# Performance work log

Measured on AMD Instinct MI355X. Metric: run time of the kernel, lower is better.

Reference implementation:

```python
import jax, jax.numpy as jnp
import numpy as np

N_SLOTS, WORD, R_HEADS = 256, 64, 4
EPS = 1e-6
IFACE = R_HEADS * WORD + 3 * WORD + 5 * R_HEADS + 3  # 471


def _oneplus(x):
    return 1.0 + jax.nn.softplus(x)


def _content_weights(M, k, beta):
    # M: (B,N,W), k: (B,H,W), beta: (B,H) -> (B,H,N) softmax over slots
    Mn = M / (jnp.linalg.norm(M, axis=-1, keepdims=True) + EPS)
    kn = k / (jnp.linalg.norm(k, axis=-1, keepdims=True) + EPS)
    sim = jnp.einsum('bnw,bhw->bhn', Mn, kn)
    return jax.nn.softmax(beta[..., None] * sim, axis=-1)


def setup_inputs() -> dict:
    key = jax.random.key(0)
    ks = jax.random.split(key, 6)
    T, B, I, H, O = 64, 16, 512, 512, 512
    nn_in = I + R_HEADS * WORD  # 768
    return {
        'x': jax.random.normal(ks[0], (T, B, I), jnp.float32),
        'W_hid': jax.random.normal(ks[1], (nn_in, H), jnp.float32) / np.sqrt(nn_in),
        'b_hid': jnp.zeros((H,), jnp.float32),
        'W_iface': jax.random.normal(ks[2], (H, IFACE), jnp.float32) / np.sqrt(H),
        'W_out': jax.random.normal(ks[3], (H, O), jnp.float32) / np.sqrt(H),
        'W_memout': jax.random.normal(ks[4], (R_HEADS * WORD, O), jnp.float32) / np.sqrt(R_HEADS * WORD),
    }


def reference(x, W_hid, b_hid, W_iface, W_out, W_memout):
    T, B, _ = x.shape
    N, Wd, R = N_SLOTS, WORD, R_HEADS
    sizes = [R * Wd, R, Wd, 1, Wd, Wd, R, 1, 1, 3 * R]
    splits = np.cumsum(sizes)[:-1]
    eye = jnp.eye(N, dtype=x.dtype)

    def step(carry, x_t):
        M, u, p, L, ww, rw, rv = carry
        nn_in = jnp.concatenate([x_t, rv.reshape(B, R * Wd)], axis=-1)
        h = jax.nn.relu(nn_in @ W_hid + b_hid)
        pre_out = h @ W_out
        iface = h @ W_iface
        rk, rb, wk, wb, ev, wv, fg, ag, wg, rm = jnp.split(iface, splits, axis=-1)
        rk = rk.reshape(B, R, Wd)
        rb = _oneplus(rb)                       # (B,R)
        wk = wk.reshape(B, 1, Wd)
        wb = _oneplus(wb)                       # (B,1)
        ev = jax.nn.sigmoid(ev)                 # (B,Wd)
        fg = jax.nn.sigmoid(fg)                 # (B,R)
        ag = jax.nn.sigmoid(ag)                 # (B,1)
        wg = jax.nn.sigmoid(wg)                 # (B,1)
        rm = jax.nn.softmax(rm.reshape(B, R, 3), axis=-1)
        # --- usage / retention ---
        ret = jnp.prod(1.0 - fg[:, :, None] * rw, axis=1)          # (B,N)
        u_new = (u + ww - u * ww) * ret
        # --- allocation via usage sort ---
        free = jnp.argsort(u_new, axis=1)                           # ascending usage
        su = jnp.take_along_axis(u_new, free, axis=1)
        cp = jnp.cumprod(jnp.concatenate([jnp.ones((B, 1), su.dtype), su[:, :-1]], axis=1), axis=1)
        a_sorted = (1.0 - su) * cp
        inv = jnp.argsort(free, axis=1)
        a = jnp.take_along_axis(a_sorted, inv, axis=1)              # (B,N)
        # --- write weighting + memory update ---
        cw = _content_weights(M, wk, wb)[:, 0]                      # (B,N)
        ww_new = wg * (ag * a + (1.0 - ag) * cw)                    # (B,N)
        M_new = M * (1.0 - ww_new[:, :, None] * ev[:, None, :]) + ww_new[:, :, None] * wv[:, None, :]
        # --- temporal link matrix ---
        L_new = (1.0 - ww_new[:, :, None] - ww_new[:, None, :]) * L + ww_new[:, :, None] * p[:, None, :]
        L_new = L_new * (1.0 - eye)
        p_new = (1.0 - jnp.sum(ww_new, axis=1, keepdims=True)) * p + ww_new
        # --- read ---
        rc = _content_weights(M_new, rk, rb)                        # (B,R,N)
        fwd = jnp.einsum('bnm,brm->brn', L_new, rw)
        bwd = jnp.einsum('bmn,brm->brn', L_new, rw)
        rw_new = rm[:, :, 0:1] * bwd + rm[:, :, 1:2] * rc + rm[:, :, 2:3] * fwd
        rv_new = jnp.einsum('bnw,brn->brw', M_new, rw_new)          # (B,R,Wd)
        out = pre_out + rv_new.reshape(B, R * Wd) @ W_memout
        return (M_new, u_new, p_new, L_new, ww_new, rw_new, rv_new), out

    init = (jnp.full((B, N, Wd), 1e-6, x.dtype),
            jnp.zeros((B, N), x.dtype),
            jnp.zeros((B, N), x.dtype),
            jnp.zeros((B, N, N), x.dtype),
            jnp.zeros((B, N), x.dtype),
            jnp.zeros((B, R, N), x.dtype),
            jnp.zeros((B, R, Wd), x.dtype))
    _, outputs = jax.lax.scan(step, init, x)
    return outputs  # (T, B, output_size)
```

## Files before the change

### kernel.cpp

```cpp
#include <hip/hip_runtime.h>
#include <math.h>

#define TS 64
#define IFACE_N 471
#define EPS_ 1e-6f

#define OFF_RK 0
#define OFF_RB 256
#define OFF_WK 260
#define OFF_WB 324
#define OFF_EV 325
#define OFF_WV 389
#define OFF_FG 453
#define OFF_AG 457
#define OFF_WG 458
#define OFF_RM 459

#define O_HX   0
#define O_RS   524288
#define O_L    1048576
#define WIPS 260
#define WHPS 132
#define O_WIP  2097152
#define O_WHP  2219612

__device__ __forceinline__ float sigmoidf_(float x){ return 1.f/(1.f+expf(-x)); }
__device__ __forceinline__ float oneplusf_(float x){ return 1.f+fmaxf(x,0.f)+log1pf(expf(-fabsf(x))); }
__device__ __forceinline__ float wsum_(float v){
#pragma unroll
  for(int off=32; off>0; off>>=1) v += __shfl_xor(v,off,64);
  return v;
}
__device__ __forceinline__ float wmax_(float v){
#pragma unroll
  for(int off=32; off>0; off>>=1) v = fmaxf(v,__shfl_xor(v,off,64));
  return v;
}
__device__ __forceinline__ unsigned bf16rne_(float f){
  unsigned u = __float_as_uint(f);
  return (u + 0x7FFFu + ((u >> 16) & 1u)) >> 16;
}
__device__ __forceinline__ unsigned bf16pack_(float lo, float hi){
  return bf16rne_(lo) | (bf16rne_(hi) << 16);
}
__device__ __forceinline__ float bflo_(unsigned p){ return __uint_as_float(p << 16); }
__device__ __forceinline__ float bfhi_(unsigned p){ return __uint_as_float(p & 0xFFFF0000u); }

__device__ __forceinline__ float dot8_(uint4 p, const float* a, float acc){
  acc = fmaf(a[0], bflo_(p.x), acc); acc = fmaf(a[1], bfhi_(p.x), acc);
  acc = fmaf(a[2], bflo_(p.y), acc); acc = fmaf(a[3], bfhi_(p.y), acc);
  acc = fmaf(a[4], bflo_(p.z), acc); acc = fmaf(a[5], bfhi_(p.z), acc);
  acc = fmaf(a[6], bflo_(p.w), acc); acc = fmaf(a[7], bfhi_(p.w), acc);
  return acc;
}

__global__ void __launch_bounds__(256) kInit(float* ws){
  int g = blockIdx.x*256 + threadIdx.x;
  for (int i=g;i<1048576;i+=65536) ws[O_L+i]=0.f;
}

__global__ void __launch_bounds__(256)
kConv(const float* __restrict__ W_hid, const float* __restrict__ W_iface,
      float* __restrict__ ws)
{
  unsigned* Wip = (unsigned*)(ws + O_WIP);
  unsigned* Whp = (unsigned*)(ws + O_WHP);
  int g = blockIdx.x*256 + threadIdx.x;
  for (int i = g; i < 471*256; i += 65536) {
    int c = i >> 8, kp = i & 255;
    Wip[c*WIPS + kp] = bf16pack_(W_iface[(size_t)(2*kp)*IFACE_N + c],
                                 W_iface[(size_t)(2*kp+1)*IFACE_N + c]);
  }
  {
    int c = g >> 7, kp = g & 127;
    Whp[c*WHPS + kp] = bf16pack_(W_hid[(size_t)(512 + 2*kp)*512 + c],
                                 W_hid[(size_t)(513 + 2*kp)*512 + c]);
  }
}

__global__ void __launch_bounds__(256)
kPre(const float* __restrict__ x, const float* __restrict__ W_hid,
     const float* __restrict__ b_hid, float* __restrict__ ws)
{
  const int tid = threadIdx.x, blk = blockIdx.x;
  const int r0 = (blk >> 1) * 8, col = (blk & 1) * 256 + tid;
  __shared__ float xs[8][512];
  for (int i = tid; i < 8*512; i += 256) {
    int rr = i >> 9, k = i & 511;
    xs[rr][k] = x[(size_t)(r0+rr)*512 + k];
  }
  __syncthreads();
  float a0=0,a1=0,a2=0,a3=0,a4=0,a5=0,a6=0,a7=0;
  const float* Wp = W_hid + col;
#pragma unroll 4
  for (int k = 0; k < 512; k++) {
    float w = Wp[(size_t)k*512];
    a0 = fmaf(xs[0][k], w, a0); a1 = fmaf(xs[1][k], w, a1);
    a2 = fmaf(xs[2][k], w, a2); a3 = fmaf(xs[3][k], w, a3);
    a4 = fmaf(xs[4][k], w, a4); a5 = fmaf(xs[5][k], w, a5);
    a6 = fmaf(xs[6][k], w, a6); a7 = fmaf(xs[7][k], w, a7);
  }
  float bh = b_hid[col];
  float av[8] = {a0,a1,a2,a3,a4,a5,a6,a7};
#pragma unroll
  for (int i = 0; i < 8; i++)
    ws[O_HX + (size_t)(r0+i)*512 + col] = av[i] + bh;
}

__global__ void __launch_bounds__(1024, 4)
kLoop(const unsigned* __restrict__ WipT, const unsigned* __restrict__ WhpT,
      float* __restrict__ hx, float* __restrict__ rvs, float* __restrict__ Lall)
{
  const int tid = threadIdx.x, b = blockIdx.x;
  const int wv = tid >> 6, lane = tid & 63;

  __shared__ float hl[512];
  __shared__ float ifcl[480];
  __shared__ float psum[1024];
  __shared__ alignas(16) float ul[256];
  __shared__ alignas(16) float pOl[256];
  __shared__ float pNl[256];
  __shared__ alignas(16) float wwl[256];
  __shared__ alignas(16) float rwl[1024];
  __shared__ float wkn[64], rknl[256];
  __shared__ alignas(16) float evl[64], wvl[64];
  __shared__ float ssorted[256];
  __shared__ int   sidx[256];
  __shared__ float sal[256], siml[256], cwl[256];
  __shared__ float fwdl[1024], bwdl[1024], rcs[1024];
  __shared__ alignas(16) float bb[16][2][260];
  __shared__ float rvl[256];
  __shared__ float sSa;
  __shared__ alignas(16) float Ml[16384];

  float* Lg = Lall + (size_t)b*65536;

  if (tid < 512) hl[tid] = fmaxf(hx[(size_t)b*512 + tid], 0.f);
  rwl[tid] = 0.f;
  if (tid < 256){ ul[tid]=0.f; pOl[tid]=0.f; wwl[tid]=0.f; }
  for (int i = tid; i < 16384; i += 1024) Ml[i] = 1e-6f;
  __syncthreads();

  for (int t = 0; t < TS; t++) {
    if (tid < 512) hx[(size_t)(t*16 + b)*512 + tid] = hl[tid];

    {
      int col = tid & 511, kseg = tid >> 9;
      float acc = 0.f;
      if (col < IFACE_N) {
        const uint4* Wp = (const uint4*)(WipT + col*WIPS + kseg*128);
        const float* hp = hl + kseg*256;
#pragma unroll 8
        for (int q4 = 0; q4 < 32; q4++) acc = dot8_(Wp[q4], hp + q4*8, acc);
      }
      psum[tid] = acc;
    }
    __syncthreads();
    if (tid < IFACE_N) ifcl[tid] = psum[tid] + psum[512+tid];
    __syncthreads();

    if (tid < 256) {
      float ret = 1.f;
#pragma unroll
      for (int r = 0; r < 4; r++) {
        float fg = sigmoidf_(ifcl[OFF_FG + r]);
        ret *= (1.f - fg * rwl[r*256 + tid]);
      }
      float uo = ul[tid], wo = wwl[tid];
      ul[tid] = (uo + wo - uo*wo) * ret;
    } else if (tid >= 448 && tid < 512) {
      float kv = ifcl[OFF_WK + lane];
      float ss = wsum_(kv*kv);
      wkn[lane] = kv / (sqrtf(ss) + EPS_);
    } else if (tid >= 512 && tid < 768) {
      int r = wv - 8;
      float kv = ifcl[OFF_RK + r*64 + lane];
      float ss = wsum_(kv*kv);
      rknl[r*64 + lane] = kv / (sqrtf(ss) + EPS_);
    } else if (tid >= 768 && tid < 832) {
      evl[lane] = sigmoidf_(ifcl[OFF_EV + lane]);
    } else if (tid >= 832 && tid < 896) {
      wvl[lane] = ifcl[OFF_WV + lane];
    }
    __syncthreads();

    {
      int n = tid >> 2, q = tid & 3;
      const float4* Mp = (const float4*)(Ml + n*64 + q*16);
      float4 m0 = Mp[0], m1 = Mp[1], m2 = Mp[2], m3 = Mp[3];
      float un = ul[n];
      const float4* sp4 = (const float4*)(ul + q*64);
      int cnt = 0;
#pragma unroll 4
      for (int m4 = 0; m4 < 16; m4++) {
        float4 um = sp4[m4];
        int gm = q*64 + m4*4;
        cnt += (um.x < un || (um.x == un && gm   < n)) ? 1 : 0;
        cnt += (um.y < un || (um.y == un && gm+1 < n)) ? 1 : 0;
        cnt += (um.z < un || (um.z == un && gm+2 < n)) ? 1 : 0;
        cnt += (um.w < un || (um.w == un && gm+3 < n)) ? 1 : 0;
      }
      cnt += __shfl_xor(cnt, 1, 64);
      cnt += __shfl_xor(cnt, 2, 64);
      const float* kp = wkn + q*16;
      float ss = m0.x*m0.x + m0.y*m0.y + m0.z*m0.z + m0.w*m0.w
               + m1.x*m1.x + m1.y*m1.y + m1.z*m1.z + m1.w*m1.w
               + m2.x*m2.x + m2.y*m2.y + m2.z*m2.z + m2.w*m2.w
               + m3.x*m3.x + m3.y*m3.y + m3.z*m3.z + m3.w*m3.w;
      float dt = m0.x*kp[0] + m0.y*kp[1] + m0.z*kp[2] + m0.w*kp[3]
               + m1.x*kp[4] + m1.y*kp[5] + m1.z*kp[6] + m1.w*kp[7]
               + m2.x*kp[8] + m2.y*kp[9] + m2.z*kp[10] + m2.w*kp[11]
               + m3.x*kp[12] + m3.y*kp[13] + m3.z*kp[14] + m3.w*kp[15];
      ss += __shfl_xor(ss,1,64); ss += __shfl_xor(ss,2,64);
      dt += __shfl_xor(dt,1,64); dt += __shfl_xor(dt,2,64);
      if (q == 0) {
        ssorted[cnt] = un; sidx[cnt] = n;
        float wb = oneplusf_(ifcl[OFF_WB]);
        siml[n] = wb * dt / (sqrtf(ss) + EPS_);
      }
    }
    __syncthreads();

    if (wv == 0) {
      float carry = 1.f;
      float s_acc = 0.f;
#pragma unroll
      for (int c2 = 0; c2 < 4; c2++) {
        float v0 = ssorted[c2*64 + lane];
        float v = v0;
#pragma unroll
        for (int off = 1; off < 64; off <<= 1) {
          float uu = __shfl_up(v, off, 64);
          if (lane >= off) v *= uu;
        }
        float e = __shfl_up(v, 1, 64);
        if (lane == 0) e = 1.f;
        float av = (1.f - v0) * e * carry;
        sal[sidx[c2*64 + lane]] = av;
        s_acc += av;
        carry *= __shfl(v, 63, 64);
      }
      float S = wsum_(s_acc);
      if (lane == 0) sSa = S;
    } else if (wv >= 4 && wv < 8) {
      int s = tid - 256;
      float v0 = siml[lane], v1 = siml[64+lane], v2 = siml[128+lane], v3 = siml[192+lane];
      float mx = wmax_(fmaxf(fmaxf(v0,v1), fmaxf(v2,v3)));
      float ssum = wsum_(expf(v0-mx)+expf(v1-mx)+expf(v2-mx)+expf(v3-mx));
      cwl[s] = expf(siml[s]-mx) / ssum;
    }
    __syncthreads();

    if (tid < 256) {
      float ag = sigmoidf_(ifcl[OFF_AG]);
      float wg = sigmoidf_(ifcl[OFF_WG]);
      float wwn = wg * (ag*sal[tid] + (1.f-ag)*cwl[tid]);
      wwl[tid] = wwn;
      float wws = wg * (ag*sSa + (1.f-ag));
      pNl[tid] = (1.f - wws)*pOl[tid] + wwn;
    }
    __syncthreads();

    {
      const int j0 = lane*4;
      const float4 wj  = *(const float4*)(wwl + j0);
      const float4 pj  = *(const float4*)(pOl + j0);
      const float4 rw0 = *(const float4*)(rwl + j0);
      const float4 rw1 = *(const float4*)(rwl + 256 + j0);
      const float4 rw2 = *(const float4*)(rwl + 512 + j0);
      const float4 rw3 = *(const float4*)(rwl + 768 + j0);
      float4 ba0 = {0,0,0,0}, ba1 = {0,0,0,0}, ba2 = {0,0,0,0}, ba3 = {0,0,0,0};
      float4* Lrow = (float4*)Lg;
#pragma unroll 4
      for (int ii = 0; ii < 16; ii++) {
        int i = wv*16 + ii;
        float wwi = wwl[i];
        float4 lv = Lrow[i*64 + lane];
        float s = 1.f - wwi;
        float4 nv;
        nv.x = (s - wj.x)*lv.x + wwi*pj.x;
        nv.y = (s - wj.y)*lv.y + wwi*pj.y;
        nv.z = (s - wj.z)*lv.z + wwi*pj.z;
        nv.w = (s - wj.w)*lv.w + wwi*pj.w;
        if (j0   == i) nv.x = 0.f;
        if (j0+1 == i) nv.y = 0.f;
        if (j0+2 == i) nv.z = 0.f;
        if (j0+3 == i) nv.w = 0.f;
        Lrow[i*64 + lane] = nv;
        float f0 = nv.x*rw0.x + nv.y*rw0.y + nv.z*rw0.z + nv.w*rw0.w;
        float f1 = nv.x*rw1.x + nv.y*rw1.y + nv.z*rw1.z + nv.w*rw1.w;
        float f2 = nv.x*rw2.x + nv.y*rw2.y + nv.z*rw2.z + nv.w*rw2.w;
        float f3 = nv.x*rw3.x + nv.y*rw3.y + nv.z*rw3.z + nv.w*rw3.w;
        float u0 = (lane & 1) ? f1 : f0;
        float v0 = (lane & 1) ? f0 : f1;
        u0 += __shfl_xor(v0, 1, 64);
        float u1 = (lane & 1) ? f3 : f2;
        float v1 = (lane & 1) ? f2 : f3;
        u1 += __shfl_xor(v1, 1, 64);
        float u2 = (lane & 2) ? u1 : u0;
        float v2 = (lane & 2) ? u0 : u1;
        u2 += __shfl_xor(v2, 2, 64);
        u2 += __shfl_xor(u2, 4, 64);
        u2 += __shfl_xor(u2, 8, 64);
        u2 += __shfl_xor(u2, 16, 64);
        u2 += __shfl_xor(u2, 32, 64);
        if (lane < 4) fwdl[lane*256 + i] = u2;
        float ri0 = rwl[i], ri1 = rwl[256+i], ri2 = rwl[512+i], ri3 = rwl[768+i];
        ba0.x = fmaf(ri0, nv.x, ba0.x); ba0.y = fmaf(ri0, nv.y, ba0.y);
        ba0.z = fmaf(ri0, nv.z, ba0.z); ba0.w = fmaf(ri0, nv.w, ba0.w);
        ba1.x = fmaf(ri1, nv.x, ba1.x); ba1.y = fmaf(ri1, nv.y, ba1.y);
        ba1.z = fmaf(ri1, nv.z, ba1.z); ba1.w = fmaf(ri1, nv.w, ba1.w);
        ba2.x = fmaf(ri2, nv.x, ba2.x); ba2.y = fmaf(ri2, nv.y, ba2.y);
        ba2.z = fmaf(ri2, nv.z, ba2.z); ba2.w = fmaf(ri2, nv.w, ba2.w);
        ba3.x = fmaf(ri3, nv.x, ba3.x); ba3.y = fmaf(ri3, nv.y, ba3.y);
        ba3.z = fmaf(ri3, nv.z, ba3.z); ba3.w = fmaf(ri3, nv.w, ba3.w);
      }
#pragma unroll
      for (int rr = 0; rr < 2; rr++) {
        float4 vA = (rr == 0) ? ba0 : ba2;
        float4 vB = (rr == 0) ? ba1 : ba3;
        *(float4*)&bb[wv][0][j0] = vA;
        *(float4*)&bb[wv][1][j0] = vB;
        __syncthreads();
        if (tid < 512) {
          int r2 = tid >> 8, col = tid & 255;
          float s = 0.f;
#pragma unroll
          for (int w2 = 0; w2 < 16; w2++) s += bb[w2][r2][col];
          bwdl[(rr*2 + r2)*256 + col] = s;
        }
        __syncthreads();
      }
    }
    if (tid < 256) pOl[tid] = pNl[tid];

    {
      int n = tid >> 2, q = tid & 3;
      float wwn = wwl[n];
      float4* Mp = (float4*)(Ml + n*64 + q*16);
      float ss = 0.f, d0 = 0.f, d1 = 0.f, d2 = 0.f, d3 = 0.f;
#pragma unroll
      for (int i = 0; i < 4; i++) {
        float4 mv = Mp[i];
        int w0 = q*16 + i*4;
        float4 ev = *(const float4*)(evl + w0);
        float4 wq = *(const float4*)(wvl + w0);
        float4 nv;
        nv.x = mv.x*(1.f - wwn*ev.x) + wwn*wq.x;
        nv.y = mv.y*(1.f - wwn*ev.y) + wwn*wq.y;
        nv.z = mv.z*(1.f - wwn*ev.z) + wwn*wq.z;
        nv.w = mv.w*(1.f - wwn*ev.w) + wwn*wq.w;
        Mp[i] = nv;
        ss += nv.x*nv.x + nv.y*nv.y + nv.z*nv.z + nv.w*nv.w;
        const float* k0 = rknl + w0;
        const float* k1 = rknl + 64 + w0;
        const float* k2 = rknl + 128 + w0;
        const float* k3 = rknl + 192 + w0;
        d0 += nv.x*k0[0] + nv.y*k0[1] + nv.z*k0[2] + nv.w*k0[3];
        d1 += nv.x*k1[0] + nv.y*k1[1] + nv.z*k1[2] + nv.w*k1[3];
        d2 += nv.x*k2[0] + nv.y*k2[1] + nv.z*k2[2] + nv.w*k2[3];
        d3 += nv.x*k3[0] + nv.y*k3[1] + nv.z*k3[2] + nv.w*k3[3];
      }
      float a  = (lane & 1) ? d1 : d0;
      float bq = (lane & 1) ? d0 : d1;
      a += __shfl_xor(bq, 1, 64);
      float c2 = (lane & 1) ? d3 : d2;
      float dq = (lane & 1) ? d2 : d3;
      c2 += __shfl_xor(dq, 1, 64);
      float e  = (lane & 2) ? c2 : a;
      float fq = (lane & 2) ? a : c2;
      e += __shfl_xor(fq, 2, 64);
      ss += __shfl_xor(ss,1,64); ss += __shfl_xor(ss,2,64);
      float inv = 1.f/(sqrtf(ss) + EPS_);
      rcs[q*256 + n] = oneplusf_(ifcl[OFF_RB + q]) * e * inv;
    }
    __syncthreads();

    if (wv < 4) {
      float* rp = rcs + wv*256;
      float v0 = rp[lane], v1 = rp[64+lane], v2 = rp[128+lane], v3 = rp[192+lane];
      float mx = wmax_(fmaxf(fmaxf(v0,v1), fmaxf(v2,v3)));
      float e0 = expf(v0-mx), e1 = expf(v1-mx), e2 = expf(v2-mx), e3 = expf(v3-mx);
      float inv = 1.f / wsum_(e0+e1+e2+e3);
      rp[lane] = e0*inv; rp[64+lane] = e1*inv; rp[128+lane] = e2*inv; rp[192+lane] = e3*inv;
    }
    __syncthreads();

    {
      int r = tid >> 8;
      float e0 = ifcl[OFF_RM + r*3+0], e1 = ifcl[OFF_RM + r*3+1], e2 = ifcl[OFF_RM + r*3+2];
      float mx = fmaxf(e0, fmaxf(e1, e2));
      float x0 = expf(e0-mx), x1 = expf(e1-mx), x2 = expf(e2-mx);
      float inv = 1.f/(x0+x1+x2);
      rwl[tid] = (x0*bwdl[tid] + x1*rcs[tid] + x2*fwdl[tid]) * inv;
    }
    __syncthreads();

    {
      int w = tid & 63, r = (tid >> 6) & 3, c = tid >> 8;
      const float* rp = rwl + r*256 + c*64;
      const float* Mp = Ml + c*4096 + w;
      float acc = 0.f;
#pragma unroll 8
      for (int n = 0; n < 64; n++) acc = fmaf(Mp[n*64], rp[n], acc);
      psum[c*256 + r*64 + w] = acc;
    }
    __syncthreads();
    if (tid < 256) {
      float v = psum[tid] + psum[256+tid] + psum[512+tid] + psum[768+tid];
      rvl[tid] = v;
      rvs[(size_t)(t*16 + b)*256 + tid] = v;
    }
    __syncthreads();

    if (t + 1 < TS) {
      int col = tid & 511, kseg = tid >> 9;
      const uint4* Wp = (const uint4*)(WhpT + col*WHPS + kseg*64);
      const float* rp = rvl + kseg*128;
      float acc = 0.f;
#pragma unroll 8
      for (int q4 = 0; q4 < 16; q4++) acc = dot8_(Wp[q4], rp + q4*8, acc);
      psum[tid] = acc;
      __syncthreads();
      if (tid < 512)
        hl[tid] = fmaxf(hx[(size_t)((t+1)*16 + b)*512 + tid] + psum[tid] + psum[512+tid], 0.f);
      __syncthreads();
    }
  }
}

__global__ void __launch_bounds__(1024)
kOut(const float* __restrict__ W_out, const float* __restrict__ W_memout,
     const float* __restrict__ hsv, const float* __restrict__ rvs,
     float* __restrict__ out)
{
  const int tid = threadIdx.x, blk = blockIdx.x;
  const int rg = blk >> 2, cq = blk & 3;
  __shared__ float hs[16*512];
  __shared__ float rs[16*256];
  for (int i = tid; i < 16*512; i += 1024) hs[i] = hsv[(size_t)rg*16*512 + i];
  for (int i = tid; i < 16*256; i += 1024) rs[i] = rvs[(size_t)rg*16*256 + i];
  __syncthreads();
  int c  = cq*128 + (tid & 127);
  int ro = tid >> 7;
  const float* h0 = hs + (2*ro)*512;
  const float* h1 = h0 + 512;
  const float* r0 = rs + (2*ro)*256;
  const float* r1 = r0 + 256;
  float a0 = 0.f, a1 = 0.f;
  const float* Wp = W_out + c;
#pragma unroll 8
  for (int k = 0; k < 512; k++) {
    float w = Wp[(size_t)k*512];
    a0 = fmaf(h0[k], w, a0);
    a1 = fmaf(h1[k], w, a1);
  }
  const float* Wm = W_memout + c;
#pragma unroll 8
  for (int k = 0; k < 256; k++) {
    float w = Wm[(size_t)k*512];
    a0 = fmaf(r0[k], w, a0);
    a1 = fmaf(r1[k], w, a1);
  }
  out[(size_t)(rg*16 + 2*ro)*512 + c]     = a0;
  out[(size_t)(rg*16 + 2*ro + 1)*512 + c] = a1;
}

extern "C" void kernel_launch(void* const* d_in, const int* in_sizes, int n_in,
                              void* d_out, int out_size, void* d_ws, size_t ws_size,
                              hipStream_t stream) {
  (void)in_sizes; (void)n_in; (void)out_size; (void)ws_size;
  const float* x        = (const float*)d_in[0];
  const float* W_hid    = (const float*)d_in[1];
  const float* b_hid    = (const float*)d_in[2];
  const float* W_iface  = (const float*)d_in[3];
  const float* W_out    = (const float*)d_in[4];
  const float* W_memout = (const float*)d_in[5];
  float* outp = (float*)d_out;
  float* ws   = (float*)d_ws;

  hipLaunchKernelGGL(kInit, dim3(256), dim3(256), 0, stream, ws);
  hipLaunchKernelGGL(kConv, dim3(256), dim3(256), 0, stream, W_hid, W_iface, ws);
  hipLaunchKernelGGL(kPre,  dim3(256), dim3(256), 0, stream, x, W_hid, b_hid, ws);

  const unsigned* WipT = (const unsigned*)(ws + O_WIP);
  const unsigned* WhpT = (const unsigned*)(ws + O_WHP);
  float* hx   = ws + O_HX;
  float* rvs  = ws + O_RS;
  float* Lall = ws + O_L;

  hipLaunchKernelGGL(kLoop, dim3(16), dim3(1024), 0, stream,
                     WipT, WhpT, hx, rvs, Lall);
  hipLaunchKernelGGL(kOut, dim3(256), dim3(1024), 0, stream,
                     W_out, W_memout, hx, rvs, outp);
}
```

Before: 2.508 ms.

## Batch forward-link shuffle reductions and overlap memory update with backward reduction

Forward-link dot products are now reduced four rows at a time using a transposing butterfly shuffle tree. That cuts the number of cross-lane shuffles per row and replaces the per-row full reduction. The memory-matrix update and content-similarity computation move into the idle upper threads during the two backward-reduction phases, which removes one barrier and overlaps the two pieces of work. The hx store is moved later in the step. This adds register pressure from the batched values, and the memory work is split across two phases of 512 threads.

```diff
diff --git a/kernel.cpp b/kernel.cpp
--- a/kernel.cpp
+++ b/kernel.cpp
@@ -142,8 +142,6 @@
   __syncthreads();
 
   for (int t = 0; t < TS; t++) {
-    if (tid < 512) hx[(size_t)(t*16 + b)*512 + tid] = hl[tid];
-
     {
       int col = tid & 511, kseg = tid >> 9;
       float acc = 0.f;
@@ -271,50 +269,71 @@
       const float4 rw3 = *(const float4*)(rwl + 768 + j0);
       float4 ba0 = {0,0,0,0}, ba1 = {0,0,0,0}, ba2 = {0,0,0,0}, ba3 = {0,0,0,0};
       float4* Lrow = (float4*)Lg;
-#pragma unroll 4
-      for (int ii = 0; ii < 16; ii++) {
-        int i = wv*16 + ii;
-        float wwi = wwl[i];
-        float4 lv = Lrow[i*64 + lane];
-        float s = 1.f - wwi;
-        float4 nv;
-        nv.x = (s - wj.x)*lv.x + wwi*pj.x;
-        nv.y = (s - wj.y)*lv.y + wwi*pj.y;
-        nv.z = (s - wj.z)*lv.z + wwi*pj.z;
-        nv.w = (s - wj.w)*lv.w + wwi*pj.w;
-        if (j0   == i) nv.x = 0.f;
-        if (j0+1 == i) nv.y = 0.f;
-        if (j0+2 == i) nv.z = 0.f;
-        if (j0+3 == i) nv.w = 0.f;
-        Lrow[i*64 + lane] = nv;
-        float f0 = nv.x*rw0.x + nv.y*rw0.y + nv.z*rw0.z + nv.w*rw0.w;
-        float f1 = nv.x*rw1.x + nv.y*rw1.y + nv.z*rw1.z + nv.w*rw1.w;
-        float f2 = nv.x*rw2.x + nv.y*rw2.y + nv.z*rw2.z + nv.w*rw2.w;
-        float f3 = nv.x*rw3.x + nv.y*rw3.y + nv.z*rw3.z + nv.w*rw3.w;
-        float u0 = (lane & 1) ? f1 : f0;
-        float v0 = (lane & 1) ? f0 : f1;
-        u0 += __shfl_xor(v0, 1, 64);
-        float u1 = (lane & 1) ? f3 : f2;
-        float v1 = (lane & 1) ? f2 : f3;
-        u1 += __shfl_xor(v1, 1, 64);
-        float u2 = (lane & 2) ? u1 : u0;
-        float v2 = (lane & 2) ? u0 : u1;
-        u2 += __shfl_xor(v2, 2, 64);
-        u2 += __shfl_xor(u2, 4, 64);
-        u2 += __shfl_xor(u2, 8, 64);
-        u2 += __shfl_xor(u2, 16, 64);
-        u2 += __shfl_xor(u2, 32, 64);
-        if (lane < 4) fwdl[lane*256 + i] = u2;
-        float ri0 = rwl[i], ri1 = rwl[256+i], ri2 = rwl[512+i], ri3 = rwl[768+i];
-        ba0.x = fmaf(ri0, nv.x, ba0.x); ba0.y = fmaf(ri0, nv.y, ba0.y);
-        ba0.z = fmaf(ri0, nv.z, ba0.z); ba0.w = fmaf(ri0, nv.w, ba0.w);
-        ba1.x = fmaf(ri1, nv.x, ba1.x); ba1.y = fmaf(ri1, nv.y, ba1.y);
-        ba1.z = fmaf(ri1, nv.z, ba1.z); ba1.w = fmaf(ri1, nv.w, ba1.w);
-        ba2.x = fmaf(ri2, nv.x, ba2.x); ba2.y = fmaf(ri2, nv.y, ba2.y);
-        ba2.z = fmaf(ri2, nv.z, ba2.z); ba2.w = fmaf(ri2, nv.w, ba2.w);
-        ba3.x = fmaf(ri3, nv.x, ba3.x); ba3.y = fmaf(ri3, nv.y, ba3.y);
-        ba3.z = fmaf(ri3, nv.z, ba3.z); ba3.w = fmaf(ri3, nv.w, ba3.w);
-      }
+#pragma unroll
+      for (int batch = 0; batch < 4; batch++) {
+        float vals[16];
+#pragma unroll
+        for (int il = 0; il < 4; il++) {
+          int i = wv*16 + batch*4 + il;
+          float wwi = wwl[i];
+          float4 lv = Lrow[i*64 + lane];
+          float s = 1.f - wwi;
+          float4 nv;
+          nv.x = (s - wj.x)*lv.x + wwi*pj.x;
+          nv.y = (s - wj.y)*lv.y + wwi*pj.y;
+          nv.z = (s - wj.z)*lv.z + wwi*pj.z;
+          nv.w = (s - wj.w)*lv.w + wwi*pj.w;
+          if (j0   == i) nv.x = 0.f;
+          if (j0+1 == i) nv.y = 0.f;
+          if (j0+2 == i) nv.z = 0.f;
+          if (j0+3 == i) nv.w = 0.f;
+          Lrow[i*64 + lane] = nv;
+          vals[il*4+0] = nv.x*rw0.x + nv.y*rw0.y + nv.z*rw0.z + nv.w*rw0.w;
+          vals[il*4+1] = nv.x*rw1.x + nv.y*rw1.y + nv.z*rw1.z + nv.w*rw1.w;
+          vals[il*4+2] = nv.x*rw2.x + nv.y*rw2.y + nv.z*rw2.z + nv.w*rw2.w;
+          vals[il*4+3] = nv.x*rw3.x + nv.y*rw3.y + nv.z*rw3.z + nv.w*rw3.w;
+          float ri0 = rwl[i], ri1 = rwl[256+i], ri2 = rwl[512+i], ri3 = rwl[768+i];
+          ba0.x = fmaf(ri0, nv.x, ba0.x); ba0.y = fmaf(ri0, nv.y, ba0.y);
+          ba0.z = fmaf(ri0, nv.z, ba0.z); ba0.w = fmaf(ri0, nv.w, ba0.w);
+          ba1.x = fmaf(ri1, nv.x, ba1.x); ba1.y = fmaf(ri1, nv.y, ba1.y);
+          ba1.z = fmaf(ri1, nv.z, ba1.z); ba1.w = fmaf(ri1, nv.w, ba1.w);
+          ba2.x = fmaf(ri2, nv.x, ba2.x); ba2.y = fmaf(ri2, nv.y, ba2.y);
+          ba2.z = fmaf(ri2, nv.z, ba2.z); ba2.w = fmaf(ri2, nv.w, ba2.w);
+          ba3.x = fmaf(ri3, nv.x, ba3.x); ba3.y = fmaf(ri3, nv.y, ba3.y);
+          ba3.z = fmaf(ri3, nv.z, ba3.z); ba3.w = fmaf(ri3, nv.w, ba3.w);
+        }
+        float m8[8], m4a[4], m2a[2], m1;
+#pragma unroll
+        for (int k = 0; k < 8; k++) {
+          float keep = (lane & 1) ? vals[2*k+1] : vals[2*k];
+          float send = (lane & 1) ? vals[2*k]   : vals[2*k+1];
+          m8[k] = keep + __shfl_xor(send, 1, 64);
+        }
+#pragma unroll
+        for (int k = 0; k < 4; k++) {
+          float keep = (lane & 2) ? m8[2*k+1] : m8[2*k];
+          float send = (lane & 2) ? m8[2*k]   : m8[2*k+1];
+          m4a[k] = keep + __shfl_xor(send, 2, 64);
+        }
+#pragma unroll
+        for (int k = 0; k < 2; k++) {
+          float keep = (lane & 4) ? m4a[2*k+1] : m4a[2*k];
+          float send = (lane & 4) ? m4a[2*k]   : m4a[2*k+1];
+          m2a[k] = keep + __shfl_xor(send, 4, 64);
+        }
+        {
+          float keep = (lane & 8) ? m2a[1] : m2a[0];
+          float send = (lane & 8) ? m2a[0] : m2a[1];
+          m1 = keep + __shfl_xor(send, 8, 64);
+        }
+        m1 += __shfl_xor(m1, 16, 64);
+        m1 += __shfl_xor(m1, 32, 64);
+        if (lane < 16)
+          fwdl[(lane & 3)*256 + (wv*16 + batch*4 + (lane >> 2))] = m1;
+      }
+
+      if (tid < 512) hx[(size_t)(t*16 + b)*512 + tid] = hl[tid];
+
 #pragma unroll
       for (int rr = 0; rr < 2; rr++) {
         float4 vA = (rr == 0) ? ba0 : ba2;
@@ -328,53 +347,51 @@
 #pragma unroll
           for (int w2 = 0; w2 < 16; w2++) s += bb[w2][r2][col];
           bwdl[(rr*2 + r2)*256 + col] = s;
+          if (rr == 1 && tid < 256) pOl[tid] = pNl[tid];
+        } else {
+          int s2 = tid - 512;
+          int n = rr*128 + (s2 >> 2), q = s2 & 3;
+          float wwn = wwl[n];
+          float4* Mp = (float4*)(Ml + n*64 + q*16);
+          float ss = 0.f, d0 = 0.f, d1 = 0.f, d2 = 0.f, d3 = 0.f;
+#pragma unroll
+          for (int i = 0; i < 4; i++) {
+            float4 mv = Mp[i];
+            int w0 = q*16 + i*4;
+            float4 ev = *(const float4*)(evl + w0);
+            float4 wq = *(const float4*)(wvl + w0);
+            float4 nv;
+            nv.x = mv.x*(1.f - wwn*ev.x) + wwn*wq.x;
+            nv.y = mv.y*(1.f - wwn*ev.y) + wwn*wq.y;
+            nv.z = mv.z*(1.f - wwn*ev.z) + wwn*wq.z;
+            nv.w = mv.w*(1.f - wwn*ev.w) + wwn*wq.w;
+            Mp[i] = nv;
+            ss += nv.x*nv.x + nv.y*nv.y + nv.z*nv.z + nv.w*nv.w;
+            const float* k0 = rknl + w0;
+            const float* k1 = rknl + 64 + w0;
+            const float* k2 = rknl + 128 + w0;
+            const float* k3 = rknl + 192 + w0;
+            d0 += nv.x*k0[0] + nv.y*k0[1] + nv.z*k0[2] + nv.w*k0[3];
+            d1 += nv.x*k1[0] + nv.y*k1[1] + nv.z*k1[2] + nv.w*k1[3];
+            d2 += nv.x*k2[0] + nv.y*k2[1] + nv.z*k2[2] + nv.w*k2[3];
+            d3 += nv.x*k3[0] + nv.y*k3[1] + nv.z*k3[2] + nv.w*k3[3];
+          }
+          float a  = (lane & 1) ? d1 : d0;
+          float bq = (lane & 1) ? d0 : d1;
+          a += __shfl_xor(bq, 1, 64);
+          float c2 = (lane & 1) ? d3 : d2;
+          float dq = (lane & 1) ? d2 : d3;
+          c2 += __shfl_xor(dq, 1, 64);
+          float e  = (lane & 2) ? c2 : a;
+          float fq = (lane & 2) ? a : c2;
+          e += __shfl_xor(fq, 2, 64);
+          ss += __shfl_xor(ss,1,64); ss += __shfl_xor(ss,2,64);
+          float inv = 1.f/(sqrtf(ss) + EPS_);
+          rcs[q*256 + n] = oneplusf_(ifcl[OFF_RB + q]) * e * inv;
         }
         __syncthreads();
       }
     }
-    if (tid < 256) pOl[tid] = pNl[tid];
-
-    {
-      int n = tid >> 2, q = tid & 3;
-      float wwn = wwl[n];
-      float4* Mp = (float4*)(Ml + n*64 + q*16);
-      float ss = 0.f, d0 = 0.f, d1 = 0.f, d2 = 0.f, d3 = 0.f;
-#pragma unroll
-      for (int i = 0; i < 4; i++) {
-        float4 mv = Mp[i];
-        int w0 = q*16 + i*4;
-        float4 ev = *(const float4*)(evl + w0);
-        float4 wq = *(const float4*)(wvl + w0);
-        float4 nv;
-        nv.x = mv.x*(1.f - wwn*ev.x) + wwn*wq.x;
-        nv.y = mv.y*(1.f - wwn*ev.y) + wwn*wq.y;
-        nv.z = mv.z*(1.f - wwn*ev.z) + wwn*wq.z;
-        nv.w = mv.w*(1.f - wwn*ev.w) + wwn*wq.w;
-        Mp[i] = nv;
-        ss += nv.x*nv.x + nv.y*nv.y + nv.z*nv.z + nv.w*nv.w;
-        const float* k0 = rknl + w0;
-        const float* k1 = rknl + 64 + w0;
-        const float* k2 = rknl + 128 + w0;
-        const float* k3 = rknl + 192 + w0;
-        d0 += nv.x*k0[0] + nv.y*k0[1] + nv.z*k0[2] + nv.w*k0[3];
-        d1 += nv.x*k1[0] + nv.y*k1[1] + nv.z*k1[2] + nv.w*k1[3];
-        d2 += nv.x*k2[0] + nv.y*k2[1] + nv.z*k2[2] + nv.w*k2[3];
-        d3 += nv.x*k3[0] + nv.y*k3[1] + nv.z*k3[2] + nv.w*k3[3];
-      }
-      float a  = (lane & 1) ? d1 : d0;
-      float bq = (lane & 1) ? d0 : d1;
-      a += __shfl_xor(bq, 1, 64);
-      float c2 = (lane & 1) ? d3 : d2;
-      float dq = (lane & 1) ? d2 : d3;
-      c2 += __shfl_xor(dq, 1, 64);
-      float e  = (lane & 2) ? c2 : a;
-      float fq = (lane & 2) ? a : c2;
-      e += __shfl_xor(fq, 2, 64);
-      ss += __shfl_xor(ss,1,64); ss += __shfl_xor(ss,2,64);
-      float inv = 1.f/(sqrtf(ss) + EPS_);
-      rcs[q*256 + n] = oneplusf_(ifcl[OFF_RB + q]) * e * inv;
-    }
-    __syncthreads();
 
     if (wv < 4) {
       float* rp = rcs + wv*256;
```

New measurement: 3.811 ms. 1.52x slower.
